# Optimization experiments

Hardware: AMD Instinct MI355X
Metric: run time of the kernel (lower is better)

Reference implementation:

```python
import jax, jax.numpy as jnp
import numpy as np

B, H, C = 1, 4, 32
D = H * C          # 128
S, L = 128, 256
EPS = 1e-5


def _axial_layer_norm(x, gamma, beta):
    # normalize over channel axis (axis=1) of [B, D, S, L]
    mu = jnp.mean(x, axis=1, keepdims=True)
    var = jnp.var(x, axis=1, keepdims=True)
    xn = (x - mu) * jax.lax.rsqrt(var + EPS)
    return xn * gamma[None, :, None, None] + beta[None, :, None, None]


def setup_inputs() -> dict:
    key = jax.random.key(0)
    ks = jax.random.split(key, 5)
    x = jax.random.normal(ks[0], (B, D, S, L), dtype=jnp.float32)
    w_row = jax.random.normal(ks[1], (3 * D, D), dtype=jnp.float32) * 0.02
    b_row = jax.random.normal(ks[2], (3 * D,), dtype=jnp.float32) * 0.02
    w_col = jax.random.normal(ks[3], (3 * D, D), dtype=jnp.float32) * 0.02
    b_col = jax.random.normal(ks[4], (3 * D,), dtype=jnp.float32) * 0.02
    return {
        "x": x,
        "w_row": w_row, "b_row": b_row,
        "w_col": w_col, "b_col": b_col,
        "gamma1": jnp.ones((D,), jnp.float32), "beta1": jnp.zeros((D,), jnp.float32),
        "gamma2": jnp.ones((D,), jnp.float32), "beta2": jnp.zeros((D,), jnp.float32),
    }


def _qkv(x, w, b):
    # 1x1 conv == channel matmul: [3D, D] x [B, D, S, L] -> [B, 3D, S, L]
    qkv = jnp.einsum('od,bdsl->bosl', w, x) + b[None, :, None, None]
    q, k, v = jnp.split(qkv, 3, axis=1)
    rs = lambda t: t.reshape(t.shape[0], H, C, S, L)
    return rs(q), rs(k), rs(v)


def reference(x, w_row, b_row, w_col, b_col, gamma1, beta1, gamma2, beta2):
    # --- row attention (attend along L within each row s) ---
    q, k, v = _qkv(x, w_row, b_row)
    row_attn = jnp.einsum('bhcsi,bhcsj->bhsij', q, k)   # [B,H,S,L,L], no 1/sqrt(d) scaling (as in source)
    row_attn = jax.nn.softmax(row_attn, axis=-1)
    row_out = jnp.einsum('bhsij,bhdsj->bhdsi', row_attn, v).reshape(x.shape[0], D, S, L)
    out = _axial_layer_norm(x + row_out, gamma1, beta1)

    # --- column attention (attend along S within each column l) ---
    q, k, v = _qkv(out, w_col, b_col)
    col_attn = jnp.einsum('bhcil,bhcjl->bhijl', q, k)   # [B,H,S,S,L]
    col_attn = jax.nn.softmax(col_attn, axis=-2)
    col_out = jnp.einsum('bhijl,bhdjl->bhdil', col_attn, v).reshape(x.shape[0], D, S, L)
    out = _axial_layer_norm(out + col_out, gamma2, beta2)
    return out
```

## Files before the change

kernel.cpp:

```cpp
#include <hip/hip_runtime.h>
#include <hip/hip_bf16.h>

#define SL     32768
#define EPS_LN 1e-5f

typedef unsigned short u16;
typedef __attribute__((ext_vector_type(8))) short bf16x8;
typedef __attribute__((ext_vector_type(4))) float f32x4;

#define MFMA16(a, b, c) __builtin_amdgcn_mfma_f32_16x16x32_bf16((a), (b), (c), 0, 0, 0)

__device__ inline u16 f2bf(float f) {
    __hip_bfloat16 h = __float2bfloat16(f);
    return *reinterpret_cast<u16*>(&h);
}
__device__ inline float bf2f(u16 u) {
    unsigned v = ((unsigned)u) << 16;
    float f;
    __builtin_memcpy(&f, &v, 4);
    return f;
}
__device__ inline uint4 pack8(float4 a, float4 b) {
    union { uint4 v; u16 u[8]; } U;
    U.u[0] = f2bf(a.x); U.u[1] = f2bf(a.y); U.u[2] = f2bf(a.z); U.u[3] = f2bf(a.w);
    U.u[4] = f2bf(b.x); U.u[5] = f2bf(b.y); U.u[6] = f2bf(b.z); U.u[7] = f2bf(b.w);
    return U.v;
}

__global__ __launch_bounds__(256) void wcast_kernel(const float* __restrict__ wr,
                                                    const float* __restrict__ wc,
                                                    u16* __restrict__ wrb,
                                                    u16* __restrict__ wcb) {
    const int i = blockIdx.x * 256 + threadIdx.x;
    const int NW = 384 * 128 / 8;
    const float* src = (i < NW) ? wr : wc;
    u16* dst = (i < NW) ? wrb : wcb;
    const int j = (i < NW) ? i : i - NW;
    float4 a = ((const float4*)src)[j * 2];
    float4 b = ((const float4*)src)[j * 2 + 1];
    ((uint4*)dst)[j] = pack8(a, b);
}

template<typename T>
__global__ __launch_bounds__(256) void qkv_mfma(const T* __restrict__ in,
                                                const u16* __restrict__ wb,
                                                const float* __restrict__ bq,
                                                u16* __restrict__ qT,
                                                u16* __restrict__ kT,
                                                u16* __restrict__ vb) {
    __shared__ u16 xT[64][136];
    __shared__ float bs[128];
    const int bid = blockIdx.x;
    const int ot = bid % 3;
    const int o0 = ot * 128;
    const int n0 = (bid / 3) * 64;
    const int t = threadIdx.x;
    const int lane = t & 63, wv = t >> 6, lo = lane & 15, hi = lane >> 4;

    bf16x8 af[2][4];
    #pragma unroll
    for (int om = 0; om < 2; ++om)
        #pragma unroll
        for (int ks = 0; ks < 4; ++ks)
            af[om][ks] = *(const bf16x8*)(wb + (size_t)(o0 + wv * 32 + om * 16 + lo) * 128
                                             + hi * 8 + ks * 32);

    #pragma unroll
    for (int itr = 0; itr < 4; ++itr) {
        const int u = t + itr * 256;
        const int d = u & 127, noct = u >> 7;
        if constexpr (sizeof(T) == 4) {
            const float* src = (const float*)in + (size_t)d * SL + n0 + noct * 8;
            float4 f0 = *(const float4*)src;
            float4 f1 = *(const float4*)(src + 4);
            xT[noct * 8 + 0][d] = f2bf(f0.x);
            xT[noct * 8 + 1][d] = f2bf(f0.y);
            xT[noct * 8 + 2][d] = f2bf(f0.z);
            xT[noct * 8 + 3][d] = f2bf(f0.w);
            xT[noct * 8 + 4][d] = f2bf(f1.x);
            xT[noct * 8 + 5][d] = f2bf(f1.y);
            xT[noct * 8 + 6][d] = f2bf(f1.z);
            xT[noct * 8 + 7][d] = f2bf(f1.w);
        } else {
            union { uint4 v; u16 s[8]; } U;
            U.v = *(const uint4*)((const u16*)in + (size_t)d * SL + n0 + noct * 8);
            #pragma unroll
            for (int j = 0; j < 8; ++j) xT[noct * 8 + j][d] = U.s[j];
        }
    }
    if (t < 128) bs[t] = bq[o0 + t];
    __syncthreads();

    u16* tbuf = (ot == 0) ? qT : kT;

    #pragma unroll
    for (int nt = 0; nt < 4; ++nt) {
        bf16x8 bfr[4];
        #pragma unroll
        for (int ks = 0; ks < 4; ++ks)
            bfr[ks] = *(const bf16x8*)&xT[nt * 16 + lo][hi * 8 + ks * 32];
        #pragma unroll
        for (int om = 0; om < 2; ++om) {
            f32x4 acc = {0.f, 0.f, 0.f, 0.f};
            #pragma unroll
            for (int ks = 0; ks < 4; ++ks)
                acc = MFMA16(af[om][ks], bfr[ks], acc);
            if (ot < 2) {
                ushort4 o4;
                o4.x = f2bf(acc[0] + bs[wv * 32 + om * 16 + hi * 4 + 0]);
                o4.y = f2bf(acc[1] + bs[wv * 32 + om * 16 + hi * 4 + 1]);
                o4.z = f2bf(acc[2] + bs[wv * 32 + om * 16 + hi * 4 + 2]);
                o4.w = f2bf(acc[3] + bs[wv * 32 + om * 16 + hi * 4 + 3]);
                *(ushort4*)(tbuf + (size_t)wv * SL * 32
                            + (size_t)(n0 + nt * 16 + lo) * 32 + om * 16 + hi * 4) = o4;
            } else {
                #pragma unroll
                for (int r = 0; r < 4; ++r) {
                    const int o = wv * 32 + om * 16 + hi * 4 + r;
                    vb[(size_t)o * SL + n0 + nt * 16 + lo] = f2bf(acc[r] + bs[o]);
                }
            }
        }
    }
}

template<int KLEN, int NTHR>
__global__ __launch_bounds__(NTHR) void attn_kernel(const u16* __restrict__ qT,
                                                    const u16* __restrict__ kT,
                                                    const u16* __restrict__ vb,
                                                    u16* __restrict__ ao) {
    constexpr int NJT = KLEN / 16;
    constexpr int NW = NTHR / 64;
    constexpr int NOUT = SL / KLEN;
    __shared__ u16 PT[NW][2][16][36];

    const int bid = blockIdx.x;
    const int outer = bid % NOUT;
    const int h = bid / NOUT;
    const int base = outer * KLEN;
    const int t = threadIdx.x;
    const int lane = t & 63, wv = t >> 6, lo = lane & 15, hi = lane >> 4;
    const int i0w = wv * 32;

    const u16* qh = qT + (size_t)h * SL * 32;
    const u16* kh = kT + (size_t)h * SL * 32;
    const u16* vh = vb + (size_t)h * 32 * SL;

    bf16x8 qf0 = *(const bf16x8*)(qh + (size_t)(base + i0w + lo) * 32 + hi * 8);
    bf16x8 qf1 = *(const bf16x8*)(qh + (size_t)(base + i0w + 16 + lo) * 32 + hi * 8);

    f32x4 o00 = {0.f, 0.f, 0.f, 0.f}, o01 = {0.f, 0.f, 0.f, 0.f};
    f32x4 o10 = {0.f, 0.f, 0.f, 0.f}, o11 = {0.f, 0.f, 0.f, 0.f};
    float ls0[4] = {0.f, 0.f, 0.f, 0.f};
    float ls1[4] = {0.f, 0.f, 0.f, 0.f};

    #pragma unroll
    for (int jt = 0; jt < NJT; ++jt) {
        bf16x8 kf = *(const bf16x8*)(kh + (size_t)(base + jt * 16 + lo) * 32 + hi * 8);
        f32x4 z = {0.f, 0.f, 0.f, 0.f};
        f32x4 s0 = MFMA16(qf0, kf, z);
        f32x4 s1 = MFMA16(qf1, kf, z);
        #pragma unroll
        for (int r = 0; r < 4; ++r) {
            float p0 = __expf(s0[r]);
            ls0[r] += p0;
            PT[wv][0][hi * 4 + r][(jt & 1) * 16 + lo] = f2bf(p0);
            float p1 = __expf(s1[r]);
            ls1[r] += p1;
            PT[wv][1][hi * 4 + r][(jt & 1) * 16 + lo] = f2bf(p1);
        }
        if (jt & 1) {
            const int jb = (jt - 1) * 16;
            bf16x8 pf0 = *(const bf16x8*)&PT[wv][0][lo][hi * 8];
            bf16x8 pf1 = *(const bf16x8*)&PT[wv][1][lo][hi * 8];
            bf16x8 v0 = *(const bf16x8*)(vh + (size_t)lo * SL + base + jb + hi * 8);
            bf16x8 v1 = *(const bf16x8*)(vh + (size_t)(16 + lo) * SL + base + jb + hi * 8);
            o00 = MFMA16(pf0, v0, o00);
            o01 = MFMA16(pf0, v1, o01);
            o10 = MFMA16(pf1, v0, o10);
            o11 = MFMA16(pf1, v1, o11);
        }
    }
    #pragma unroll
    for (int r = 0; r < 4; ++r) {
        float v0 = ls0[r];
        v0 += __shfl_xor(v0, 1);
        v0 += __shfl_xor(v0, 2);
        v0 += __shfl_xor(v0, 4);
        v0 += __shfl_xor(v0, 8);
        ls0[r] = 1.f / v0;
        float v1 = ls1[r];
        v1 += __shfl_xor(v1, 1);
        v1 += __shfl_xor(v1, 2);
        v1 += __shfl_xor(v1, 4);
        v1 += __shfl_xor(v1, 8);
        ls1[r] = 1.f / v1;
    }
    {
        ushort4 o4;
        o4.x = f2bf(o00[0] * ls0[0]);
        o4.y = f2bf(o00[1] * ls0[1]);
        o4.z = f2bf(o00[2] * ls0[2]);
        o4.w = f2bf(o00[3] * ls0[3]);
        *(ushort4*)(ao + (size_t)(h * 32 + lo) * SL + base + i0w + hi * 4) = o4;
        o4.x = f2bf(o01[0] * ls0[0]);
        o4.y = f2bf(o01[1] * ls0[1]);
        o4.z = f2bf(o01[2] * ls0[2]);
        o4.w = f2bf(o01[3] * ls0[3]);
        *(ushort4*)(ao + (size_t)(h * 32 + 16 + lo) * SL + base + i0w + hi * 4) = o4;
        o4.x = f2bf(o10[0] * ls1[0]);
        o4.y = f2bf(o10[1] * ls1[1]);
        o4.z = f2bf(o10[2] * ls1[2]);
        o4.w = f2bf(o10[3] * ls1[3]);
        *(ushort4*)(ao + (size_t)(h * 32 + lo) * SL + base + i0w + 16 + hi * 4) = o4;
        o4.x = f2bf(o11[0] * ls1[0]);
        o4.y = f2bf(o11[1] * ls1[1]);
        o4.z = f2bf(o11[2] * ls1[2]);
        o4.w = f2bf(o11[3] * ls1[3]);
        *(ushort4*)(ao + (size_t)(h * 32 + 16 + lo) * SL + base + i0w + 16 + hi * 4) = o4;
    }
}

template<int NIN, typename T0, typename TO>
__global__ __launch_bounds__(256) void ln_fused(const T0* __restrict__ in0,
                                                const u16* __restrict__ in1,
                                                const float* __restrict__ g,
                                                const float* __restrict__ be,
                                                TO* __restrict__ outp) {
    constexpr int NOUT = SL / NIN;
    constexpr int CT = NIN / 16;
    __shared__ float val[128][69];
    __shared__ float redS[4][72];
    __shared__ float redQ[4][72];
    __shared__ float stat[64][2];
    const int bid = blockIdx.x;
    const int r0 = (bid / CT) * 4;
    const int c0 = (bid % CT) * 16;
    const int t = threadIdx.x;
    const int pos = t & 63, q = t >> 6;
    const size_t gp = (size_t)(r0 + (pos >> 4)) * NIN + c0 + (pos & 15);

    float s = 0.f, ss = 0.f;
    #pragma unroll 4
    for (int dd = 0; dd < 32; ++dd) {
        const int d = q * 32 + dd;
        float v;
        if constexpr (sizeof(T0) == 4) v = ((const float*)in0)[(size_t)d * SL + gp];
        else                           v = bf2f(((const u16*)in0)[(size_t)d * SL + gp]);
        v += bf2f(in1[(size_t)d * SL + gp]);
        val[d][pos] = v;
        s += v; ss += v * v;
    }
    redS[q][pos] = s;
    redQ[q][pos] = ss;
    __syncthreads();
    if (t < 64) {
        const float S  = redS[0][t] + redS[1][t] + redS[2][t] + redS[3][t];
        const float SS = redQ[0][t] + redQ[1][t] + redQ[2][t] + redQ[3][t];
        const float mean = S * (1.f / 128.f);
        const float var  = SS * (1.f / 128.f) - mean * mean;
        stat[t][0] = mean;
        stat[t][1] = rsqrtf(var + EPS_LN);
    }
    __syncthreads();

    {
        const int d = t >> 1;
        const int ch = (t & 1) * 8;
        const float gd = g[d], bd = be[d];
        #pragma unroll
        for (int cc = 0; cc < 8; ++cc) {
            const int c = ch + cc;
            float ov[4];
            #pragma unroll
            for (int r = 0; r < 4; ++r) {
                const int p = r * 16 + c;
                ov[r] = (val[d][p] - stat[p][0]) * stat[p][1] * gd + bd;
            }
            if constexpr (sizeof(TO) == 4) {
                float* dst = (float*)outp + (size_t)d * SL + (c0 + c) * NOUT + r0;
                *(float4*)dst = make_float4(ov[0], ov[1], ov[2], ov[3]);
            } else {
                u16* dst = (u16*)outp + (size_t)d * SL + (c0 + c) * NOUT + r0;
                ushort4 o4;
                o4.x = f2bf(ov[0]); o4.y = f2bf(ov[1]);
                o4.z = f2bf(ov[2]); o4.w = f2bf(ov[3]);
                *(ushort4*)dst = o4;
            }
        }
    }
}

extern "C" void kernel_launch(void* const* d_in, const int* in_sizes, int n_in,
                              void* d_out, int out_size, void* d_ws, size_t ws_size,
                              hipStream_t stream) {
    const float* x     = (const float*)d_in[0];
    const float* w_row = (const float*)d_in[1];
    const float* b_row = (const float*)d_in[2];
    const float* w_col = (const float*)d_in[3];
    const float* b_col = (const float*)d_in[4];
    const float* g1    = (const float*)d_in[5];
    const float* be1   = (const float*)d_in[6];
    const float* g2    = (const float*)d_in[7];
    const float* be2   = (const float*)d_in[8];
    float* out = (float*)d_out;

    char* base = (char*)d_ws;
    u16* qTb = (u16*)base;                        base += (size_t)128 * SL * 2;
    u16* kTb = (u16*)base;                        base += (size_t)128 * SL * 2;
    u16* vbb = (u16*)base;                        base += (size_t)128 * SL * 2;
    u16* ao16 = (u16*)base;                       base += (size_t)128 * SL * 2;
    u16* o1b  = (u16*)base;                       base += (size_t)128 * SL * 2;
    u16* wrb  = (u16*)base;                       base += (size_t)384 * 128 * 2;
    u16* wcb  = (u16*)base;

    wcast_kernel<<<48, 256, 0, stream>>>(w_row, w_col, wrb, wcb);
    qkv_mfma<float><<<1536, 256, 0, stream>>>(x, wrb, b_row, qTb, kTb, vbb);
    attn_kernel<256, 512><<<512, 512, 0, stream>>>(qTb, kTb, vbb, ao16);
    ln_fused<256, float, u16><<<512, 256, 0, stream>>>(x, ao16, g1, be1, o1b);
    qkv_mfma<u16><<<1536, 256, 0, stream>>>(o1b, wcb, b_col, qTb, kTb, vbb);
    attn_kernel<128, 256><<<1024, 256, 0, stream>>>(qTb, kTb, vbb, ao16);
    ln_fused<128, u16, float><<<512, 256, 0, stream>>>(o1b, ao16, g2, be2, out);
}
```

Before: 107.0 us.

## Fuse weight cast into QKV kernel and store mid LN output channel-last

Removes the separate weight-cast kernel; each QKV block now converts its fp32 weight fragments to bf16 on load. The intermediate layer-norm output is written in a position-major, channel-contiguous layout, so the second QKV projection can load 16-byte rows directly without a scattered transpose into shared memory. The final LN reads that layout with vector loads. The cost is redundant weight conversion in every block (1536 blocks) and different write patterns in ln_mid.

```diff
diff --git a/kernel.cpp b/kernel.cpp
--- a/kernel.cpp
+++ b/kernel.cpp
@@ -20,30 +20,10 @@
     __builtin_memcpy(&f, &v, 4);
     return f;
 }
-__device__ inline uint4 pack8(float4 a, float4 b) {
-    union { uint4 v; u16 u[8]; } U;
-    U.u[0] = f2bf(a.x); U.u[1] = f2bf(a.y); U.u[2] = f2bf(a.z); U.u[3] = f2bf(a.w);
-    U.u[4] = f2bf(b.x); U.u[5] = f2bf(b.y); U.u[6] = f2bf(b.z); U.u[7] = f2bf(b.w);
-    return U.v;
-}
-
-__global__ __launch_bounds__(256) void wcast_kernel(const float* __restrict__ wr,
-                                                    const float* __restrict__ wc,
-                                                    u16* __restrict__ wrb,
-                                                    u16* __restrict__ wcb) {
-    const int i = blockIdx.x * 256 + threadIdx.x;
-    const int NW = 384 * 128 / 8;
-    const float* src = (i < NW) ? wr : wc;
-    u16* dst = (i < NW) ? wrb : wcb;
-    const int j = (i < NW) ? i : i - NW;
-    float4 a = ((const float4*)src)[j * 2];
-    float4 b = ((const float4*)src)[j * 2 + 1];
-    ((uint4*)dst)[j] = pack8(a, b);
-}
-
-template<typename T>
-__global__ __launch_bounds__(256) void qkv_mfma(const T* __restrict__ in,
-                                                const u16* __restrict__ wb,
+
+template<int LAYOUT>
+__global__ __launch_bounds__(256) void qkv_mfma(const void* __restrict__ inv,
+                                                const float* __restrict__ wq,
                                                 const float* __restrict__ bq,
                                                 u16* __restrict__ qT,
                                                 u16* __restrict__ kT,
@@ -61,16 +41,23 @@
     #pragma unroll
     for (int om = 0; om < 2; ++om)
         #pragma unroll
-        for (int ks = 0; ks < 4; ++ks)
-            af[om][ks] = *(const bf16x8*)(wb + (size_t)(o0 + wv * 32 + om * 16 + lo) * 128
-                                             + hi * 8 + ks * 32);
-
-    #pragma unroll
-    for (int itr = 0; itr < 4; ++itr) {
-        const int u = t + itr * 256;
-        const int d = u & 127, noct = u >> 7;
-        if constexpr (sizeof(T) == 4) {
-            const float* src = (const float*)in + (size_t)d * SL + n0 + noct * 8;
+        for (int ks = 0; ks < 4; ++ks) {
+            const float* src = wq + (size_t)(o0 + wv * 32 + om * 16 + lo) * 128
+                                  + hi * 8 + ks * 32;
+            float4 a = *(const float4*)src;
+            float4 b = *(const float4*)(src + 4);
+            union { bf16x8 v; u16 u[8]; } U;
+            U.u[0] = f2bf(a.x); U.u[1] = f2bf(a.y); U.u[2] = f2bf(a.z); U.u[3] = f2bf(a.w);
+            U.u[4] = f2bf(b.x); U.u[5] = f2bf(b.y); U.u[6] = f2bf(b.z); U.u[7] = f2bf(b.w);
+            af[om][ks] = U.v;
+        }
+
+    if constexpr (LAYOUT == 0) {
+        #pragma unroll
+        for (int itr = 0; itr < 4; ++itr) {
+            const int u = t + itr * 256;
+            const int d = u & 127, noct = u >> 7;
+            const float* src = (const float*)inv + (size_t)d * SL + n0 + noct * 8;
             float4 f0 = *(const float4*)src;
             float4 f1 = *(const float4*)(src + 4);
             xT[noct * 8 + 0][d] = f2bf(f0.x);
@@ -81,11 +68,14 @@
             xT[noct * 8 + 5][d] = f2bf(f1.y);
             xT[noct * 8 + 6][d] = f2bf(f1.z);
             xT[noct * 8 + 7][d] = f2bf(f1.w);
-        } else {
-            union { uint4 v; u16 s[8]; } U;
-            U.v = *(const uint4*)((const u16*)in + (size_t)d * SL + n0 + noct * 8);
-            #pragma unroll
-            for (int j = 0; j < 8; ++j) xT[noct * 8 + j][d] = U.s[j];
+        }
+    } else {
+        #pragma unroll
+        for (int itr = 0; itr < 4; ++itr) {
+            const int u = t + itr * 256;
+            const int n = u >> 4, seg = u & 15;
+            *(uint4*)&xT[n][seg * 8] =
+                *(const uint4*)((const u16*)inv + (size_t)(n0 + n) * 128 + seg * 8);
         }
     }
     if (t < 128) bs[t] = bq[o0 + t];
@@ -221,35 +211,90 @@
     }
 }
 
-template<int NIN, typename T0, typename TO>
-__global__ __launch_bounds__(256) void ln_fused(const T0* __restrict__ in0,
-                                                const u16* __restrict__ in1,
-                                                const float* __restrict__ g,
-                                                const float* __restrict__ be,
-                                                TO* __restrict__ outp) {
-    constexpr int NOUT = SL / NIN;
-    constexpr int CT = NIN / 16;
+__global__ __launch_bounds__(256) void ln_mid(const float* __restrict__ in0,
+                                              const u16* __restrict__ in1,
+                                              const float* __restrict__ g,
+                                              const float* __restrict__ be,
+                                              u16* __restrict__ outp) {
+    __shared__ float val[128][69];
+    __shared__ float redS[4][72];
+    __shared__ float redQ[4][72];
+    __shared__ float stat[64][2];
+    __shared__ float gs[128], bes[128];
+    const int bid = blockIdx.x;
+    const int r0 = (bid / 16) * 4;
+    const int c0 = (bid % 16) * 16;
+    const int t = threadIdx.x;
+    const int pos = t & 63, q = t >> 6;
+    const size_t gp = (size_t)(r0 + (pos >> 4)) * 256 + c0 + (pos & 15);
+
+    if (t < 128) { gs[t] = g[t]; bes[t] = be[t]; }
+    float s = 0.f, ss = 0.f;
+    #pragma unroll 4
+    for (int dd = 0; dd < 32; ++dd) {
+        const int d = q * 32 + dd;
+        float v = in0[(size_t)d * SL + gp] + bf2f(in1[(size_t)d * SL + gp]);
+        val[d][pos] = v;
+        s += v; ss += v * v;
+    }
+    redS[q][pos] = s;
+    redQ[q][pos] = ss;
+    __syncthreads();
+    if (t < 64) {
+        const float S  = redS[0][t] + redS[1][t] + redS[2][t] + redS[3][t];
+        const float SS = redQ[0][t] + redQ[1][t] + redQ[2][t] + redQ[3][t];
+        const float mean = S * (1.f / 128.f);
+        const float var  = SS * (1.f / 128.f) - mean * mean;
+        stat[t][0] = mean;
+        stat[t][1] = rsqrtf(var + EPS_LN);
+    }
+    __syncthreads();
+
+    {
+        const int pr = pos >> 4, pc = pos & 15;
+        const size_t pp = (size_t)(c0 + pc) * 128 + r0 + pr;
+        const float mean = stat[pos][0], rstd = stat[pos][1];
+        union { uint4 v[4]; u16 u[32]; } O;
+        #pragma unroll
+        for (int dd = 0; dd < 32; ++dd) {
+            const int d = q * 32 + dd;
+            O.u[dd] = f2bf((val[d][pos] - mean) * rstd * gs[d] + bes[d]);
+        }
+        uint4* dst = (uint4*)(outp + pp * 128 + q * 32);
+        #pragma unroll
+        for (int k = 0; k < 4; ++k) dst[k] = O.v[k];
+    }
+}
+
+__global__ __launch_bounds__(256) void ln_out(const u16* __restrict__ in0,
+                                              const u16* __restrict__ in1,
+                                              const float* __restrict__ g,
+                                              const float* __restrict__ be,
+                                              float* __restrict__ outp) {
     __shared__ float val[128][69];
     __shared__ float redS[4][72];
     __shared__ float redQ[4][72];
     __shared__ float stat[64][2];
     const int bid = blockIdx.x;
-    const int r0 = (bid / CT) * 4;
-    const int c0 = (bid % CT) * 16;
+    const int r0 = (bid / 8) * 4;
+    const int c0 = (bid % 8) * 16;
     const int t = threadIdx.x;
     const int pos = t & 63, q = t >> 6;
-    const size_t gp = (size_t)(r0 + (pos >> 4)) * NIN + c0 + (pos & 15);
+    const size_t gp = (size_t)(r0 + (pos >> 4)) * 128 + c0 + (pos & 15);
 
     float s = 0.f, ss = 0.f;
-    #pragma unroll 4
-    for (int dd = 0; dd < 32; ++dd) {
-        const int d = q * 32 + dd;
-        float v;
-        if constexpr (sizeof(T0) == 4) v = ((const float*)in0)[(size_t)d * SL + gp];
-        else                           v = bf2f(((const u16*)in0)[(size_t)d * SL + gp]);
-        v += bf2f(in1[(size_t)d * SL + gp]);
-        val[d][pos] = v;
-        s += v; ss += v * v;
+    {
+        union { uint4 v[4]; u16 u[32]; } A;
+        const uint4* src = (const uint4*)(in0 + gp * 128 + q * 32);
+        #pragma unroll
+        for (int k = 0; k < 4; ++k) A.v[k] = src[k];
+        #pragma unroll 4
+        for (int dd = 0; dd < 32; ++dd) {
+            const int d = q * 32 + dd;
+            float v = bf2f(A.u[dd]) + bf2f(in1[(size_t)d * SL + gp]);
+            val[d][pos] = v;
+            s += v; ss += v * v;
+        }
     }
     redS[q][pos] = s;
     redQ[q][pos] = ss;
@@ -277,16 +322,8 @@
                 const int p = r * 16 + c;
                 ov[r] = (val[d][p] - stat[p][0]) * stat[p][1] * gd + bd;
             }
-            if constexpr (sizeof(TO) == 4) {
-                float* dst = (float*)outp + (size_t)d * SL + (c0 + c) * NOUT + r0;
-                *(float4*)dst = make_float4(ov[0], ov[1], ov[2], ov[3]);
-            } else {
-                u16* dst = (u16*)outp + (size_t)d * SL + (c0 + c) * NOUT + r0;
-                ushort4 o4;
-                o4.x = f2bf(ov[0]); o4.y = f2bf(ov[1]);
-                o4.z = f2bf(ov[2]); o4.w = f2bf(ov[3]);
-                *(ushort4*)dst = o4;
-            }
+            float* dst = outp + (size_t)d * SL + (c0 + c) * 256 + r0;
+            *(float4*)dst = make_float4(ov[0], ov[1], ov[2], ov[3]);
         }
     }
 }
@@ -310,15 +347,12 @@
     u16* kTb = (u16*)base;                        base += (size_t)128 * SL * 2;
     u16* vbb = (u16*)base;                        base += (size_t)128 * SL * 2;
     u16* ao16 = (u16*)base;                       base += (size_t)128 * SL * 2;
-    u16* o1b  = (u16*)base;                       base += (size_t)128 * SL * 2;
-    u16* wrb  = (u16*)base;                       base += (size_t)384 * 128 * 2;
-    u16* wcb  = (u16*)base;
-
-    wcast_kernel<<<48, 256, 0, stream>>>(w_row, w_col, wrb, wcb);
-    qkv_mfma<float><<<1536, 256, 0, stream>>>(x, wrb, b_row, qTb, kTb, vbb);
+    u16* o1b  = (u16*)base;
+
+    qkv_mfma<0><<<1536, 256, 0, stream>>>(x, w_row, b_row, qTb, kTb, vbb);
     attn_kernel<256, 512><<<512, 512, 0, stream>>>(qTb, kTb, vbb, ao16);
-    ln_fused<256, float, u16><<<512, 256, 0, stream>>>(x, ao16, g1, be1, o1b);
-    qkv_mfma<u16><<<1536, 256, 0, stream>>>(o1b, wcb, b_col, qTb, kTb, vbb);
+    ln_mid<<<512, 256, 0, stream>>>(x, ao16, g1, be1, o1b);
+    qkv_mfma<1><<<1536, 256, 0, stream>>>(o1b, w_col, b_col, qTb, kTb, vbb);
     attn_kernel<128, 256><<<1024, 256, 0, stream>>>(qTb, kTb, vbb, ao16);
-    ln_fused<128, u16, float><<<512, 256, 0, stream>>>(o1b, ao16, g2, be2, out);
-}
+    ln_out<<<512, 256, 0, stream>>>(o1b, ao16, g2, be2, out);
+}
```

After: 110.7 us. 1.03x slower.
